# Performance work log

Hardware: AMD Instinct MI355X
Metric: run time of the kernel (lower is better)

## Reference

```python
import jax, jax.numpy as jnp
import numpy as np

OUT_H, OUT_W = 512, 512  # output_size init kwarg


def setup_inputs() -> dict:
    key = jax.random.key(0)
    k1, k2, k3 = jax.random.split(key, 3)
    X = jax.random.normal(k1, (16, 512, 512, 16), dtype=jnp.float32)
    scale = jax.random.uniform(k2, (16, 1), dtype=jnp.float32)
    translate = jax.random.normal(k3, (16, 2), dtype=jnp.float32)
    return {"X": X, "scale": scale, "translate": translate}


def reference(X, scale, translate):
    B, H, W, C = X.shape
    # build per-batch 2x3 affine: [[s, 0, tx], [0, s, ty]]
    s = scale[:, 0]
    z = jnp.zeros_like(s)
    theta = jnp.stack([s, z, translate[:, 0], z, s, translate[:, 1]], axis=1).reshape(B, 2, 3)

    # regular grid in [-1, 1], homogeneous coords: [3, N], N = OUT_H*OUT_W
    x_lin = jnp.linspace(-1.0, 1.0, OUT_W)
    y_lin = jnp.linspace(-1.0, 1.0, OUT_H)
    xc, yc = jnp.meshgrid(x_lin, y_lin)  # each [OUT_H, OUT_W], 'xy' indexing as in tf.meshgrid
    grid = jnp.stack([xc.ravel(), yc.ravel(), jnp.ones(OUT_H * OUT_W, dtype=jnp.float32)], axis=0)

    # sampled grid: [B, 2, N]
    sg = jnp.einsum('bij,jn->bin', theta, grid)
    # map from [-1,1] to pixel coords; original multiplies by W (not W-1) -- keep faithful
    x = 0.5 * (sg[:, 0, :] + 1.0) * W  # [B, N]
    y = 0.5 * (sg[:, 1, :] + 1.0) * H

    # corner indices: TF cast truncates toward zero, as does astype(int32)
    x0 = x.astype(jnp.int32)
    x1 = x0 + 1
    y0 = y.astype(jnp.int32)
    y1 = y0 + 1
    x0 = jnp.clip(x0, 0, W - 1)
    x1 = jnp.clip(x1, 0, W - 1)
    y0 = jnp.clip(y0, 0, H - 1)
    y1 = jnp.clip(y1, 0, H - 1)

    # gather 4 neighbors: [B, N, C]
    b = jnp.arange(B)[:, None]
    pa = X[b, y0, x0]
    pb = X[b, y1, x0]
    pc = X[b, y0, x1]
    pd = X[b, y1, x1]

    # bilinear weights use the clipped integer corners recast to float (as original)
    x0f = x0.astype(x.dtype)
    x1f = x1.astype(x.dtype)
    y0f = y0.astype(y.dtype)
    y1f = y1.astype(y.dtype)
    wa = ((x1f - x) * (y1f - y))[..., None]
    wb = ((x1f - x) * (y - y0f))[..., None]
    wc = ((x - x0f) * (y1f - y))[..., None]
    wd = ((x - x0f) * (y - y0f))[..., None]

    out = wa * pa + wb * pb + wc * pc + wd * pd  # [B, N, C]
    return out.reshape(B, OUT_H, OUT_W, C)
```

## Files before the change

### kernel.cpp

```cpp
#include <hip/hip_runtime.h>


#define BH   512
#define BW   512
#define BC   16
#define NB   16
#define HALF 256
#define WMAX 264
#define NXCD 8

typedef float f32x4 __attribute__((ext_vector_type(4)));

__device__ __forceinline__ int swz(int x_local, int q) {
    return (x_local << 2) | (q ^ ((x_local >> 1) & 3));
}

__global__ __launch_bounds__(256) void bilerp_kernel(
    const float* __restrict__ X,
    const float* __restrict__ scale,
    const float* __restrict__ translate,
    float* __restrict__ out)
{
    __shared__ float4 lds[2][WMAX * 4];

    const int nwg_per_xcd = (NB * BH * 2) / NXCD;
    const int wid = (blockIdx.x % NXCD) * nwg_per_xcd + blockIdx.x / NXCD;

    const int b    = wid >> 10;
    const int i    = (wid >> 1) & 511;
    const int half = wid & 1;

    const float s  = scale[b];
    const float tx = translate[2 * b];
    const float ty = translate[2 * b + 1];

    const float yl = -1.0f + 2.0f * (float)i / 511.0f;
    const float y  = 0.5f * (s * yl + ty + 1.0f) * (float)BH;
    int y0 = (int)y;
    int y1 = y0 + 1;
    y0 = min(max(y0, 0), BH - 1);
    y1 = min(max(y1, 0), BH - 1);
    const float wy1 = (float)y1 - y;
    const float wy0 = y - (float)y0;

    const int jbase = half * HALF;
    const float xl_f = -1.0f + 2.0f * (float)jbase / 511.0f;
    const float xl_e = -1.0f + 2.0f * (float)(jbase + HALF - 1) / 511.0f;
    const float x_f  = 0.5f * (s * xl_f + tx + 1.0f) * (float)BW;
    const float x_e  = 0.5f * (s * xl_e + tx + 1.0f) * (float)BW;
    const int x0_f = (int)x_f;
    const int x0_e = (int)x_e;
    const int mlo = min(x0_f, x0_e);
    const int mhi = max(x0_f, x0_e) + 1;
    const int xlo = min(max(mlo, 0), BW - 1);
    const int xhi = min(max(mhi, 0), BW - 1);
    int width = xhi - xlo + 1;
    if (width > WMAX) width = WMAX;

    const float4* __restrict__ Xb = (const float4*)(X + (size_t)b * BH * BW * BC);
    const float4* __restrict__ g0 = Xb + (size_t)y0 * (BW * (BC / 4)) + xlo * 4;
    const float4* __restrict__ g1 = Xb + (size_t)y1 * (BW * (BC / 4)) + xlo * 4;
    const int nf4 = width * 4;
    for (int t = threadIdx.x; t < nf4; t += 256) {
        const int dst = swz(t >> 2, t & 3);
        lds[0][dst] = g0[t];
        lds[1][dst] = g1[t];
    }
    __syncthreads();

    f32x4* __restrict__ orow =
        (f32x4*)out + (size_t)(b * BH + i) * (BW * (BC / 4));

    const int tid = threadIdx.x;
    const int q   = tid & 3;
    const int p0  = tid >> 2;

    #pragma unroll
    for (int k = 0; k < 4; ++k) {
        const int j = jbase + p0 + 64 * k;
        const float xl = -1.0f + 2.0f * (float)j / 511.0f;
        const float x  = 0.5f * (s * xl + tx + 1.0f) * (float)BW;
        int x0 = (int)x;
        int x1 = x0 + 1;
        x0 = min(max(x0, 0), BW - 1);
        x1 = min(max(x1, 0), BW - 1);
        const float wx1 = (float)x1 - x;
        const float wx0 = x - (float)x0;

        const float wa = wx1 * wy1;
        const float wb = wx1 * wy0;
        const float wc = wx0 * wy1;
        const float wd = wx0 * wy0;

        const int i0 = swz(x0 - xlo, q);
        const int i1 = swz(x1 - xlo, q);
        const float4 pa = lds[0][i0];
        const float4 pb = lds[1][i0];
        const float4 pc = lds[0][i1];
        const float4 pd = lds[1][i1];

        f32x4 o;
        o.x = wa * pa.x + wb * pb.x + wc * pc.x + wd * pd.x;
        o.y = wa * pa.y + wb * pb.y + wc * pc.y + wd * pd.y;
        o.z = wa * pa.z + wb * pb.z + wc * pc.z + wd * pd.z;
        o.w = wa * pa.w + wb * pb.w + wc * pc.w + wd * pd.w;

        __builtin_nontemporal_store(o, &orow[j * 4 + q]);
    }
}

extern "C" void kernel_launch(void* const* d_in, const int* in_sizes, int n_in,
                              void* d_out, int out_size, void* d_ws, size_t ws_size,
                              hipStream_t stream) {
    const float* X         = (const float*)d_in[0];
    const float* scale     = (const float*)d_in[1];
    const float* translate = (const float*)d_in[2];
    float* out             = (float*)d_out;

    dim3 grid(NB * BH * 2);
    dim3 block(256);
    bilerp_kernel<<<grid, block, 0, stream>>>(X, scale, translate, out);
}
```

Measured before the change: 413.3 us.

## Drop LDS staging and gather neighbors directly from global memory per output row

Removes the shared-memory staging of the two source rows (with swizzle and barrier) and reads the four bilinear neighbors straight from global memory, relying on the caches for reuse. Each workgroup now covers a full 512-pixel output row instead of half a row, so the grid is halved and each thread loops over eight output pixels. This removes the LDS writes, the barrier and the duplicated edge loads between halves, at the cost of more global and cache traffic for neighbors shared by adjacent outputs, plus fewer workgroups to hide latency.

```diff
diff --git a/kernel.cpp b/kernel.cpp
--- a/kernel.cpp
+++ b/kernel.cpp
@@ -5,15 +5,9 @@
 #define BW   512
 #define BC   16
 #define NB   16
-#define HALF 256
-#define WMAX 264
 #define NXCD 8
 
 typedef float f32x4 __attribute__((ext_vector_type(4)));
-
-__device__ __forceinline__ int swz(int x_local, int q) {
-    return (x_local << 2) | (q ^ ((x_local >> 1) & 3));
-}
 
 __global__ __launch_bounds__(256) void bilerp_kernel(
     const float* __restrict__ X,
@@ -21,14 +15,11 @@
     const float* __restrict__ translate,
     float* __restrict__ out)
 {
-    __shared__ float4 lds[2][WMAX * 4];
+    const int nper = (NB * BH) / NXCD;
+    const int blk  = (blockIdx.x % NXCD) * nper + blockIdx.x / NXCD;
 
-    const int nwg_per_xcd = (NB * BH * 2) / NXCD;
-    const int wid = (blockIdx.x % NXCD) * nwg_per_xcd + blockIdx.x / NXCD;
-
-    const int b    = wid >> 10;
-    const int i    = (wid >> 1) & 511;
-    const int half = wid & 1;
+    const int b = blk >> 9;
+    const int i = blk & 511;
 
     const float s  = scale[b];
     const float tx = translate[2 * b];
@@ -43,41 +34,17 @@
     const float wy1 = (float)y1 - y;
     const float wy0 = y - (float)y0;
 
-    const int jbase = half * HALF;
-    const float xl_f = -1.0f + 2.0f * (float)jbase / 511.0f;
-    const float xl_e = -1.0f + 2.0f * (float)(jbase + HALF - 1) / 511.0f;
-    const float x_f  = 0.5f * (s * xl_f + tx + 1.0f) * (float)BW;
-    const float x_e  = 0.5f * (s * xl_e + tx + 1.0f) * (float)BW;
-    const int x0_f = (int)x_f;
-    const int x0_e = (int)x_e;
-    const int mlo = min(x0_f, x0_e);
-    const int mhi = max(x0_f, x0_e) + 1;
-    const int xlo = min(max(mlo, 0), BW - 1);
-    const int xhi = min(max(mhi, 0), BW - 1);
-    int width = xhi - xlo + 1;
-    if (width > WMAX) width = WMAX;
-
-    const float4* __restrict__ Xb = (const float4*)(X + (size_t)b * BH * BW * BC);
-    const float4* __restrict__ g0 = Xb + (size_t)y0 * (BW * (BC / 4)) + xlo * 4;
-    const float4* __restrict__ g1 = Xb + (size_t)y1 * (BW * (BC / 4)) + xlo * 4;
-    const int nf4 = width * 4;
-    for (int t = threadIdx.x; t < nf4; t += 256) {
-        const int dst = swz(t >> 2, t & 3);
-        lds[0][dst] = g0[t];
-        lds[1][dst] = g1[t];
-    }
-    __syncthreads();
-
-    f32x4* __restrict__ orow =
-        (f32x4*)out + (size_t)(b * BH + i) * (BW * (BC / 4));
+    const float4* __restrict__ Xb   = (const float4*)(X + (size_t)b * BH * BW * BC);
+    const float4* __restrict__ row0 = Xb + (size_t)y0 * (BW * (BC / 4));
+    const float4* __restrict__ row1 = Xb + (size_t)y1 * (BW * (BC / 4));
+    f32x4* __restrict__ orow = (f32x4*)out + (size_t)blk * (BW * (BC / 4));
 
     const int tid = threadIdx.x;
     const int q   = tid & 3;
     const int p0  = tid >> 2;
 
     #pragma unroll
-    for (int k = 0; k < 4; ++k) {
-        const int j = jbase + p0 + 64 * k;
+    for (int j = p0; j < BW; j += 64) {
         const float xl = -1.0f + 2.0f * (float)j / 511.0f;
         const float x  = 0.5f * (s * xl + tx + 1.0f) * (float)BW;
         int x0 = (int)x;
@@ -92,12 +59,10 @@
         const float wc = wx0 * wy1;
         const float wd = wx0 * wy0;
 
-        const int i0 = swz(x0 - xlo, q);
-        const int i1 = swz(x1 - xlo, q);
-        const float4 pa = lds[0][i0];
-        const float4 pb = lds[1][i0];
-        const float4 pc = lds[0][i1];
-        const float4 pd = lds[1][i1];
+        const float4 pa = row0[x0 * 4 + q];
+        const float4 pb = row1[x0 * 4 + q];
+        const float4 pc = row0[x1 * 4 + q];
+        const float4 pd = row1[x1 * 4 + q];
 
         f32x4 o;
         o.x = wa * pa.x + wb * pb.x + wc * pc.x + wd * pd.x;
@@ -117,7 +82,7 @@
     const float* translate = (const float*)d_in[2];
     float* out             = (float*)d_out;
 
-    dim3 grid(NB * BH * 2);
+    dim3 grid(NB * BH);
     dim3 block(256);
     bilerp_kernel<<<grid, block, 0, stream>>>(X, scale, translate, out);
 }
```

Measured after the change: 426.0 us. 1.03x slower.
